# Kernel optimization log

Hardware: AMD Instinct MI355X
Metric: run time of the kernel (lower is better)

## Reference

```python
import jax, jax.numpy as jnp
import numpy as np

NUM_EMBEDDINGS = 1024
EMBEDDING_DIM = 256
COMMITMENT_COST = 0.25
B, C, T = 16, 256, 4096


def setup_inputs() -> dict:
    key = jax.random.key(0)
    k_in, k_cb = jax.random.split(key)
    inputs = jax.random.normal(k_in, (B, C, T), dtype=jnp.float32)
    # matches nn.Embedding init uniform_(-1/K, 1/K)
    codebook = jax.random.uniform(
        k_cb, (NUM_EMBEDDINGS, EMBEDDING_DIM), dtype=jnp.float32,
        minval=-1.0 / NUM_EMBEDDINGS, maxval=1.0 / NUM_EMBEDDINGS)
    return {"inputs": inputs, "codebook": codebook}


def reference(inputs, codebook):
    # inputs: [B, C, T] -> [B, T, C] (channel-last), eval mode (no dead-code swap)
    x = jnp.transpose(inputs, (0, 2, 1))            # [B, T, C]
    flat = x.reshape(-1, EMBEDDING_DIM)             # [N, D]
    distances = (jnp.sum(flat * flat, axis=1, keepdims=True)
                 + jnp.sum(codebook * codebook, axis=1)
                 - 2.0 * jnp.matmul(flat, codebook.T))   # [N, K]
    encoding_indices = jnp.argmin(distances, axis=1)     # [N]
    quantized = codebook[encoding_indices].reshape(x.shape)  # [B, T, C]
    sg = jax.lax.stop_gradient
    e_latent_loss = jnp.mean(jnp.square(sg(quantized) - x))
    q_latent_loss = jnp.mean(jnp.square(quantized - sg(x)))
    vq_loss = e_latent_loss + COMMITMENT_COST * q_latent_loss
    quantized_st = x + sg(quantized - x)                 # straight-through
    quantized_st = jnp.transpose(quantized_st, (0, 2, 1))  # back to [B, C, T]
    indices = encoding_indices.reshape(B, T)
    return quantized_st, vq_loss, indices
```

## Files before the change

kernel.cpp:

```cpp
#include <hip/hip_runtime.h>
#include <stdint.h>

#define DIMS 256
#define NT 4096
#define NROWS 65536
#define THETA 1.5e-4f

typedef float    f32x4_t __attribute__((ext_vector_type(4)));
typedef _Float16 f16x8_t __attribute__((ext_vector_type(8)));
typedef _Float16 f16x4_t __attribute__((ext_vector_type(4)));

__global__ __launch_bounds__(64) void vq_prep(const float* __restrict__ cb,
                                              float* __restrict__ se,
                                              _Float16* __restrict__ cb16){
  __shared__ float sq[256];
  const int k = blockIdx.x;
  const int tid = threadIdx.x;
  float4 v = *(const float4*)(cb + (size_t)k*256 + tid*4);
  f16x4_t p;
  p.x = (_Float16)(v.x * 512.f);
  p.y = (_Float16)(v.y * 512.f);
  p.z = (_Float16)(v.z * 512.f);
  p.w = (_Float16)(v.w * 512.f);
  *(f16x4_t*)(cb16 + (size_t)k*256 + tid*4) = p;
  sq[tid*4+0] = __fmul_rn(v.x, v.x);
  sq[tid*4+1] = __fmul_rn(v.y, v.y);
  sq[tid*4+2] = __fmul_rn(v.z, v.z);
  sq[tid*4+3] = __fmul_rn(v.w, v.w);
  __syncthreads();
  if (tid < 16){
    const int h = tid >> 3, j = tid & 7;
    float r = sq[h*128 + j];
    #pragma unroll
    for (int i = 1; i < 16; ++i) r = __fadd_rn(r, sq[h*128 + j + 8*i]);
    r = __fadd_rn(r, __shfl_xor(r, 1));
    r = __fadd_rn(r, __shfl_xor(r, 2));
    r = __fadd_rn(r, __shfl_xor(r, 4));
    r = __fadd_rn(r, __shfl_xor(r, 8));
    if (tid == 0) se[k] = r;
  }
}


#define AH(r,c)    Ah[(size_t)(r)*264 + (c)]
#define BHL(s,k,c) Bh[((size_t)((s)*256 + (k)))*40 + (c)]
#define QQ(t,c)    q[(size_t)(t)*260 + (c)]

#define T2I(v, i, v1, i1, v2) { \
  bool lt = (v) < (v1); \
  (v2) = lt ? (v1) : fminf((v2), (v)); \
  (i1) = lt ? (i) : (i1); \
  (v1) = lt ? (v) : (v1); }

#define DECL_T2(M,R) \
  float b1_##M##R = 3.4e38f, b2_##M##R = 3.4e38f; int bi_##M##R = 0x7fffffff;

#define FOLD(M,R) { \
  float v; \
  v = fmaf(a##M##0[R], NEGI, ec0); T2I(v, kb +  0, b1_##M##R, bi_##M##R, b2_##M##R); \
  v = fmaf(a##M##1[R], NEGI, ec1); T2I(v, kb + 16, b1_##M##R, bi_##M##R, b2_##M##R); \
  v = fmaf(a##M##2[R], NEGI, ec2); T2I(v, kb + 32, b1_##M##R, bi_##M##R, b2_##M##R); \
  v = fmaf(a##M##3[R], NEGI, ec3); T2I(v, kb + 48, b1_##M##R, bi_##M##R, b2_##M##R); }

#define BSTEP(CC, S) { \
  *(f16x8_t*)&BHL((CC)&1, codeS, cOff)     = rb##S##0; \
  *(f16x8_t*)&BHL((CC)&1, codeS, cOff + 8) = rb##S##1; \
  asm volatile("s_waitcnt lgkmcnt(0)" ::: "memory"); \
  __builtin_amdgcn_s_barrier(); \
  asm volatile("" ::: "memory"); \
  { \
    const int nn = ktb + (CC) + 2; \
    if (nn < 32){ \
      const _Float16* p_ = cb16 + ((size_t)((nn>>3)*256) + codeS)*DIMS + (nn&7)*32 + cOff; \
      rb##S##0 = *(const f16x8_t*)(p_); rb##S##1 = *(const f16x8_t*)(p_ + 8); \
    } \
  } \
  { \
    f16x8_t bh0 = *(const f16x8_t*)&BHL((CC)&1, bC0, fq8); \
    f16x8_t bh1 = *(const f16x8_t*)&BHL((CC)&1, bC1, fq8); \
    f16x8_t bh2 = *(const f16x8_t*)&BHL((CC)&1, bC2, fq8); \
    f16x8_t bh3 = *(const f16x8_t*)&BHL((CC)&1, bC3, fq8); \
    f16x8_t ah0 = *(const f16x8_t*)&AH(wr32 + fr, (CC)*32 + fq8); \
    f16x8_t ah1 = *(const f16x8_t*)&AH(wr32 + 16 + fr, (CC)*32 + fq8); \
    a00 = __builtin_amdgcn_mfma_f32_16x16x32_f16(ah0, bh0, a00, 0, 0, 0); \
    a01 = __builtin_amdgcn_mfma_f32_16x16x32_f16(ah0, bh1, a01, 0, 0, 0); \
    a02 = __builtin_amdgcn_mfma_f32_16x16x32_f16(ah0, bh2, a02, 0, 0, 0); \
    a03 = __builtin_amdgcn_mfma_f32_16x16x32_f16(ah0, bh3, a03, 0, 0, 0); \
    a10 = __builtin_amdgcn_mfma_f32_16x16x32_f16(ah1, bh0, a10, 0, 0, 0); \
    a11 = __builtin_amdgcn_mfma_f32_16x16x32_f16(ah1, bh1, a11, 0, 0, 0); \
    a12 = __builtin_amdgcn_mfma_f32_16x16x32_f16(ah1, bh2, a12, 0, 0, 0); \
    a13 = __builtin_amdgcn_mfma_f32_16x16x32_f16(ah1, bh3, a13, 0, 0, 0); \
  } }

#define MSTEP(MK) { \
  float ov1 = __shfl_xor(v1, MK); int oi1 = __shfl_xor(i1, MK); float ov2 = __shfl_xor(v2, MK); \
  bool tk = ov1 < v1; \
  v2 = tk ? fminf(v1, ov2) : fminf(v2, ov1); \
  i1 = tk ? oi1 : i1; \
  v1 = tk ? ov1 : v1; }

#define MERGE(M,R) { \
  float v1 = b1_##M##R, v2 = b2_##M##R; int i1 = bi_##M##R; \
  MSTEP(1) MSTEP(2) MSTEP(4) MSTEP(8) \
  if (fr == 0) comb[(wr32 + (M)*16 + fq*4 + (R))*4 + wc] = make_float4(v1, __int_as_float(i1), v2, 0.f); }

__global__ __launch_bounds__(512, 1) void vq_scores(
    const float* __restrict__ x, const float* __restrict__ cb,
    const _Float16* __restrict__ cb16, const float* __restrict__ se,
    float* __restrict__ out0, float* __restrict__ out2,
    unsigned* __restrict__ wl, unsigned* __restrict__ cnt, double* __restrict__ accd)
{
  __shared__ __align__(16) char smem[79360];
  _Float16* Ah   = (_Float16*)smem;
  _Float16* Bh   = (_Float16*)(smem + 33792);
  float4*   comb = (float4*)(smem + 74752);
  int*      codeL= (int*)(smem + 78848);
  float*    sxa  = (float*)(smem + 79104);
  float*    q    = (float*)smem;

  const int tid  = threadIdx.x;
  const int lane = tid & 63;
  const int wid  = tid >> 6;
  const int wr   = wid >> 2;
  const int wc   = wid & 3;
  const int fr   = lane & 15;
  const int fq   = lane >> 4;
  const int wr32 = wr * 32;
  const int fq8  = fq * 8;
  const int wcfr = wc*64 + fr;
  const int n0   = blockIdx.x * 64;
  const int bb   = n0 >> 12;
  const int t0   = n0 & 4095;
  const float NEGI = -1.0f/256.0f;

  const int codeS = tid >> 1;
  const int cOff  = (tid & 1) << 4;

  f16x8_t rbA0, rbA1, rbB0, rbB1;
  {
    const _Float16* p_ = cb16 + (size_t)codeS * DIMS + cOff;
    rbA0 = *(const f16x8_t*)(p_); rbA1 = *(const f16x8_t*)(p_ + 8);
  }
  {
    const _Float16* p_ = cb16 + (size_t)codeS * DIMS + 32 + cOff;
    rbB0 = *(const f16x8_t*)(p_); rbB1 = *(const f16x8_t*)(p_ + 8);
  }

  {
    const int dup = tid >> 7;
    const int c4  = tid & 7;
    const int tt  = ((tid >> 3) & 15) << 2;
    #pragma unroll
    for (int cc2 = 0; cc2 < 2; ++cc2){
      const int c0 = (dup*2 + cc2) * 32;
      const float* xp = x + ((size_t)(bb*DIMS + c0 + c4*4))*NT + t0 + tt;
      f32x4_t va0 = __builtin_nontemporal_load((const f32x4_t*)(xp));
      f32x4_t va1 = __builtin_nontemporal_load((const f32x4_t*)(xp + NT));
      f32x4_t va2 = __builtin_nontemporal_load((const f32x4_t*)(xp + 2*NT));
      f32x4_t va3 = __builtin_nontemporal_load((const f32x4_t*)(xp + 3*NT));
      #pragma unroll
      for (int j = 0; j < 4; ++j){
        f16x4_t p;
        p.x = (_Float16)(va0[j]);
        p.y = (_Float16)(va1[j]);
        p.z = (_Float16)(va2[j]);
        p.w = (_Float16)(va3[j]);
        *(f16x4_t*)&AH(tt + j, c0 + c4*4) = p;
      }
    }
  }

  const f32x4_t Z = {0.f, 0.f, 0.f, 0.f};
  f32x4_t a00=Z,a01=Z,a02=Z,a03=Z, a10=Z,a11=Z,a12=Z,a13=Z;
  DECL_T2(0,0) DECL_T2(0,1) DECL_T2(0,2) DECL_T2(0,3)
  DECL_T2(1,0) DECL_T2(1,1) DECL_T2(1,2) DECL_T2(1,3)

  const int bC0 = wc*64 + 0*16 + fr;
  const int bC1 = wc*64 + 1*16 + fr;
  const int bC2 = wc*64 + 2*16 + fr;
  const int bC3 = wc*64 + 3*16 + fr;

  for (int kt = 0; kt < 4; ++kt){
    const int ktb = kt * 8;
    BSTEP(0,A) BSTEP(1,B) BSTEP(2,A) BSTEP(3,B)
    BSTEP(4,A) BSTEP(5,B) BSTEP(6,A) BSTEP(7,B)

    const int kb = kt*256 + wcfr;
    const float ec0 = se[kb], ec1 = se[kb+16], ec2 = se[kb+32], ec3 = se[kb+48];
    FOLD(0,0) FOLD(0,1) FOLD(0,2) FOLD(0,3)
    FOLD(1,0) FOLD(1,1) FOLD(1,2) FOLD(1,3)
    a00=Z;a01=Z;a02=Z;a03=Z; a10=Z;a11=Z;a12=Z;a13=Z;
  }

  MERGE(0,0) MERGE(0,1) MERGE(0,2) MERGE(0,3)
  MERGE(1,0) MERGE(1,1) MERGE(1,2) MERGE(1,3)
  __syncthreads();

  {
    const int row = tid >> 3, seg = tid & 7;
    float s = 0.f;
    #pragma unroll
    for (int k = 0; k < 4; ++k){
      f16x8_t hv = *(const f16x8_t*)&AH(row, seg*32 + k*8);
      #pragma unroll
      for (int e = 0; e < 8; ++e){
        float f = (float)hv[e];
        s = fmaf(f, f, s);
      }
    }
    s += __shfl_xor(s, 1);
    s += __shfl_xor(s, 2);
    s += __shfl_xor(s, 4);
    if (seg == 0) sxa[row] = s;
  }
  __syncthreads();

  if (tid < 64){
    float4 p = comb[tid*4 + 0];
    float v1 = p.x, v2 = p.z;
    int   i1 = __float_as_int(p.y);
    #pragma unroll
    for (int w = 1; w < 4; ++w){
      p = comb[tid*4 + w];
      bool tk = p.x < v1;
      v2 = tk ? fminf(v1, p.z) : fminf(v2, p.x);
      i1 = tk ? __float_as_int(p.y) : i1;
      v1 = tk ? p.x : v1;
    }
    const int r = n0 + tid;
    codeL[tid] = i1;
    out2[r] = (float)i1;
    bool flg = !(v2 - v1 >= THETA);
    if (flg){
      unsigned pos = atomicAdd(cnt, 1u);
      wl[pos] = (unsigned)r;
    }
    double c = flg ? 0.0 : (double)(sxa[tid] + v1);
    #pragma unroll
    for (int m = 1; m < 64; m <<= 1) c += __shfl_xor(c, m);
    if (tid == 0) atomicAdd(accd, c);
  }
  __syncthreads();

  {
    const int r = tid >> 3, seg = tid & 7;
    const float* src = cb + (size_t)codeL[r] * DIMS;
    #pragma unroll
    for (int k = 0; k < 8; ++k){
      float4 v = *(const float4*)(src + k*32 + seg*4);
      *(float4*)&QQ(r, k*32 + seg*4) = v;
    }
  }
  __syncthreads();

  {
    #pragma unroll
    for (int jj = 0; jj < 2; ++jj){
      const int c = wid*32 + jj*16 + (lane >> 2);
      float* dst = out0 + ((size_t)(bb*256 + c))*NT + t0;
      #pragma unroll
      for (int ii = 0; ii < 4; ++ii){
        const int tl = ii*16 + (lane & 3)*4;
        f32x4_t v;
        v[0] = QQ(tl + 0, c);
        v[1] = QQ(tl + 1, c);
        v[2] = QQ(tl + 2, c);
        v[3] = QQ(tl + 3, c);
        __builtin_nontemporal_store(v, (f32x4_t*)(dst + tl));
      }
    }
  }
}

__global__ __launch_bounds__(256) void vq_refine(
    const float* __restrict__ x, const float* __restrict__ cb,
    const float* __restrict__ se,
    const unsigned* __restrict__ wl, const unsigned* __restrict__ cnt,
    float* __restrict__ out2, float* __restrict__ out0, double* __restrict__ accd)
{
  __shared__ float eT[8][1024];
  __shared__ float xs[DIMS][8];
  __shared__ int   rows_s[8];
  __shared__ float sxs[8];
  __shared__ float wv[4][8];
  __shared__ int   wi[4][8];
  __shared__ int   wiF[8];

  const unsigned n = *cnt;
  const unsigned groups = (n + 7u) >> 3;
  const int tid  = threadIdx.x;
  const int lane = tid & 63;
  const int wid  = tid >> 6;

  for (unsigned g = blockIdx.x; g < groups; g += gridDim.x){
    __syncthreads();
    if (tid < 8){
      unsigned e = g*8u + (unsigned)tid;
      rows_s[tid] = (int)wl[e < n ? e : (n - 1u)];
    }
    __syncthreads();
    #pragma unroll
    for (int rep = 0; rep < 8; ++rep){
      int id = rep * 256 + tid;
      int c = id >> 3, r = id & 7;
      int row = rows_s[r];
      xs[c][r] = x[((size_t)((row >> 12)*DIMS + c))*NT + (row & 4095)];
    }
    __syncthreads();
    if (tid < 128){
      const int r = tid >> 4, hj = tid & 15;
      const int h = hj >> 3, j = hj & 7;
      float v0 = xs[h*128 + j][r];
      float s = __fmul_rn(v0, v0);
      #pragma unroll
      for (int i = 1; i < 16; ++i){
        float v = xs[h*128 + j + 8*i][r];
        s = __fadd_rn(s, __fmul_rn(v, v));
      }
      s = __fadd_rn(s, __shfl_xor(s, 1));
      s = __fadd_rn(s, __shfl_xor(s, 2));
      s = __fadd_rn(s, __shfl_xor(s, 4));
      s = __fadd_rn(s, __shfl_xor(s, 8));
      if (hj == 0) sxs[r] = s;
    }

    float s[8][4];
    #pragma unroll
    for (int r = 0; r < 8; ++r)
      #pragma unroll
      for (int u = 0; u < 4; ++u) s[r][u] = 0.f;

    for (int c0 = 0; c0 < DIMS; c0 += 8){
      __syncthreads();
      #pragma unroll
      for (int rep = 0; rep < 8; ++rep){
        int id2 = rep * 256 + tid;
        int k = id2 >> 1, qq = id2 & 1;
        float4 v = *(const float4*)&cb[(size_t)k * DIMS + c0 + qq * 4];
        eT[qq*4 + 0][k] = v.x; eT[qq*4 + 1][k] = v.y;
        eT[qq*4 + 2][k] = v.z; eT[qq*4 + 3][k] = v.w;
      }
      __syncthreads();
      #pragma unroll
      for (int cc = 0; cc < 8; ++cc){
        float4 ev = *(const float4*)&eT[cc][wid*256 + lane*4];
        #pragma unroll
        for (int r = 0; r < 8; ++r){
          float xv = xs[c0 + cc][r];
          s[r][0] = fmaf(xv, ev.x, s[r][0]);
          s[r][1] = fmaf(xv, ev.y, s[r][1]);
          s[r][2] = fmaf(xv, ev.z, s[r][2]);
          s[r][3] = fmaf(xv, ev.w, s[r][3]);
        }
      }
    }

    float4 sek = *(const float4*)&se[wid*256 + lane*4];
    #pragma unroll
    for (int r = 0; r < 8; ++r){
      const float sxv = sxs[r];
      float bv = 3.4e38f; int bi = 0x7fffffff;
      #pragma unroll
      for (int u = 0; u < 4; ++u){
        float d = __fsub_rn(__fadd_rn(sxv, (&sek.x)[u]),
                            __fadd_rn(s[r][u], s[r][u]));
        int k = wid*256 + lane*4 + u;
        if (d < bv || (d == bv && k < bi)) { bv = d; bi = k; }
      }
      #pragma unroll
      for (int m = 1; m < 64; m <<= 1){
        float ov = __shfl_xor(bv, m);
        int   oi = __shfl_xor(bi, m);
        if (ov < bv || (ov == bv && oi < bi)) { bv = ov; bi = oi; }
      }
      if (lane == 0){ wv[wid][r] = bv; wi[wid][r] = bi; }
    }
    __syncthreads();
    if (tid < 8){
      const int r = tid;
      float bv = wv[0][r]; int bi = wi[0][r];
      #pragma unroll
      for (int w = 1; w < 4; ++w){
        float ov = wv[w][r]; int oi = wi[w][r];
        if (ov < bv || (ov == bv && oi < bi)) { bv = ov; bi = oi; }
      }
      wiF[r] = bi;
      if (g*8u + (unsigned)r < n){
        int row = rows_s[r];
        out2[row] = (float)bi;
        atomicAdd(accd, (double)bv);
      }
    }
    __syncthreads();
    #pragma unroll
    for (int r = 0; r < 8; ++r){
      if (g*8u + (unsigned)r < n){
        int row  = rows_s[r];
        int code = wiF[r];
        out0[((size_t)((row >> 12)*256 + tid))*NT + (row & 4095)] = cb[(size_t)code*DIMS + tid];
      }
    }
  }
}

__global__ void vq_final(const double* __restrict__ accd, float* __restrict__ out1){
  *out1 = (float)(1.25 * (*accd) * (1.0 / 16777216.0));
}

extern "C" void kernel_launch(void* const* d_in, const int* in_sizes, int n_in,
                              void* d_out, int out_size, void* d_ws, size_t ws_size,
                              hipStream_t stream)
{
  const float* x  = (const float*)d_in[0];
  const float* cb = (const float*)d_in[1];
  float* out  = (float*)d_out;
  float* out0 = out;
  float* out1 = out + (size_t)16777216;
  float* out2 = out + (size_t)16777217;

  char* ws = (char*)d_ws;
  double*   accd = (double*)(ws + 0);
  unsigned* cnt  = (unsigned*)(ws + 8);
  float*    se   = (float*)(ws + 64);
  unsigned* wl   = (unsigned*)(ws + 4160);
  _Float16* cb16 = (_Float16*)(ws + 266304);

  hipMemsetAsync(d_ws, 0, 16, stream);
  vq_prep  <<<dim3(1024), dim3(64),  0, stream>>>(cb, se, cb16);
  vq_scores<<<dim3(1024), dim3(512), 0, stream>>>(x, cb, cb16, se, out0, out2, wl, cnt, accd);
  vq_refine<<<dim3(512),  dim3(256), 0, stream>>>(x, cb, se, wl, cnt, out2, out0, accd);
  vq_final <<<dim3(1),    dim3(1),   0, stream>>>(accd, out1);
}
```

Baseline: 174.2 us.

## Stream codebook tiles into LDS via global_load_lds with XOR swizzle

Replaces the register-staged codebook pipeline (global load to VGPRs, then ds_write) with direct global-to-LDS DMA loads using an XOR-swizzled, unpadded layout. This shrinks the shared-memory footprint and removes the per-step LDS store plus lgkmcnt wait. The loop becomes a single 32-step loop with a vmcnt wait and barrier per step, and s_setprio raises priority around the MFMA block. The comb buffer is pre-initialised, which adds an extra barrier, and correctness depends on the swizzle and per-wave destination mapping lining up.

```diff
diff --git a/kernel.cpp b/kernel.cpp
--- a/kernel.cpp
+++ b/kernel.cpp
@@ -9,6 +9,10 @@
 typedef float    f32x4_t __attribute__((ext_vector_type(4)));
 typedef _Float16 f16x8_t __attribute__((ext_vector_type(8)));
 typedef _Float16 f16x4_t __attribute__((ext_vector_type(4)));
+
+#define GLDS16(gsrc, ldst) \
+  __builtin_amdgcn_global_load_lds((const __attribute__((address_space(1))) void*)(gsrc), \
+      (__attribute__((address_space(3))) void*)(ldst), 16, 0, 0)
 
 __global__ __launch_bounds__(64) void vq_prep(const float* __restrict__ cb,
                                               float* __restrict__ se,
@@ -43,7 +47,6 @@
 
 
 #define AH(r,c)    Ah[(size_t)(r)*264 + (c)]
-#define BHL(s,k,c) Bh[((size_t)((s)*256 + (k)))*40 + (c)]
 #define QQ(t,c)    q[(size_t)(t)*260 + (c)]
 
 #define T2I(v, i, v1, i1, v2) { \
@@ -62,36 +65,6 @@
   v = fmaf(a##M##2[R], NEGI, ec2); T2I(v, kb + 32, b1_##M##R, bi_##M##R, b2_##M##R); \
   v = fmaf(a##M##3[R], NEGI, ec3); T2I(v, kb + 48, b1_##M##R, bi_##M##R, b2_##M##R); }
 
-#define BSTEP(CC, S) { \
-  *(f16x8_t*)&BHL((CC)&1, codeS, cOff)     = rb##S##0; \
-  *(f16x8_t*)&BHL((CC)&1, codeS, cOff + 8) = rb##S##1; \
-  asm volatile("s_waitcnt lgkmcnt(0)" ::: "memory"); \
-  __builtin_amdgcn_s_barrier(); \
-  asm volatile("" ::: "memory"); \
-  { \
-    const int nn = ktb + (CC) + 2; \
-    if (nn < 32){ \
-      const _Float16* p_ = cb16 + ((size_t)((nn>>3)*256) + codeS)*DIMS + (nn&7)*32 + cOff; \
-      rb##S##0 = *(const f16x8_t*)(p_); rb##S##1 = *(const f16x8_t*)(p_ + 8); \
-    } \
-  } \
-  { \
-    f16x8_t bh0 = *(const f16x8_t*)&BHL((CC)&1, bC0, fq8); \
-    f16x8_t bh1 = *(const f16x8_t*)&BHL((CC)&1, bC1, fq8); \
-    f16x8_t bh2 = *(const f16x8_t*)&BHL((CC)&1, bC2, fq8); \
-    f16x8_t bh3 = *(const f16x8_t*)&BHL((CC)&1, bC3, fq8); \
-    f16x8_t ah0 = *(const f16x8_t*)&AH(wr32 + fr, (CC)*32 + fq8); \
-    f16x8_t ah1 = *(const f16x8_t*)&AH(wr32 + 16 + fr, (CC)*32 + fq8); \
-    a00 = __builtin_amdgcn_mfma_f32_16x16x32_f16(ah0, bh0, a00, 0, 0, 0); \
-    a01 = __builtin_amdgcn_mfma_f32_16x16x32_f16(ah0, bh1, a01, 0, 0, 0); \
-    a02 = __builtin_amdgcn_mfma_f32_16x16x32_f16(ah0, bh2, a02, 0, 0, 0); \
-    a03 = __builtin_amdgcn_mfma_f32_16x16x32_f16(ah0, bh3, a03, 0, 0, 0); \
-    a10 = __builtin_amdgcn_mfma_f32_16x16x32_f16(ah1, bh0, a10, 0, 0, 0); \
-    a11 = __builtin_amdgcn_mfma_f32_16x16x32_f16(ah1, bh1, a11, 0, 0, 0); \
-    a12 = __builtin_amdgcn_mfma_f32_16x16x32_f16(ah1, bh2, a12, 0, 0, 0); \
-    a13 = __builtin_amdgcn_mfma_f32_16x16x32_f16(ah1, bh3, a13, 0, 0, 0); \
-  } }
-
 #define MSTEP(MK) { \
   float ov1 = __shfl_xor(v1, MK); int oi1 = __shfl_xor(i1, MK); float ov2 = __shfl_xor(v2, MK); \
   bool tk = ov1 < v1; \
@@ -110,12 +83,12 @@
     float* __restrict__ out0, float* __restrict__ out2,
     unsigned* __restrict__ wl, unsigned* __restrict__ cnt, double* __restrict__ accd)
 {
-  __shared__ __align__(16) char smem[79360];
+  __shared__ __align__(16) char smem[71168];
   _Float16* Ah   = (_Float16*)smem;
-  _Float16* Bh   = (_Float16*)(smem + 33792);
-  float4*   comb = (float4*)(smem + 74752);
-  int*      codeL= (int*)(smem + 78848);
-  float*    sxa  = (float*)(smem + 79104);
+  char*     BhRaw= smem + 33792;
+  float4*   comb = (float4*)(smem + 66560);
+  int*      codeL= (int*)(smem + 70656);
+  float*    sxa  = (float*)(smem + 70912);
   float*    q    = (float*)smem;
 
   const int tid  = threadIdx.x;
@@ -133,18 +106,25 @@
   const int t0   = n0 & 4095;
   const float NEGI = -1.0f/256.0f;
 
-  const int codeS = tid >> 1;
-  const int cOff  = (tid & 1) << 4;
-
-  f16x8_t rbA0, rbA1, rbB0, rbB1;
-  {
-    const _Float16* p_ = cb16 + (size_t)codeS * DIMS + cOff;
-    rbA0 = *(const f16x8_t*)(p_); rbA1 = *(const f16x8_t*)(p_ + 8);
-  }
-  {
-    const _Float16* p_ = cb16 + (size_t)codeS * DIMS + 32 + cOff;
-    rbB0 = *(const f16x8_t*)(p_); rbB1 = *(const f16x8_t*)(p_ + 8);
-  }
+  const int cA = wid*32 + (lane >> 2);
+  const int cB = cA + 16;
+  const int qA = (lane & 3) ^ ((cA >> 1) & 3);
+  const int qB = (lane & 3) ^ ((cB >> 1) & 3);
+  const char* cbB = (const char*)cb16;
+  const size_t srcA = (size_t)cA*512 + qA*16;
+  const size_t srcB = (size_t)cB*512 + qB*16;
+  char* dstA = BhRaw + wid*2048;
+  char* dstB = dstA + 1024;
+
+  int bOff[4];
+  #pragma unroll
+  for (int cf = 0; cf < 4; ++cf){
+    const int cd = wc*64 + cf*16 + fr;
+    bOff[cf] = cd*64 + ((fq ^ ((cd >> 1) & 3)) << 4);
+  }
+
+  GLDS16(cbB + srcA, dstA);
+  GLDS16(cbB + srcB, dstB);
 
   {
     const int dup = tid >> 7;
@@ -169,27 +149,55 @@
       }
     }
   }
+  comb[(tid >> 2)*4 + (tid & 3)] = make_float4(3.4e38f, __int_as_float(0x7fffffff), 3.4e38f, 0.f);
 
   const f32x4_t Z = {0.f, 0.f, 0.f, 0.f};
   f32x4_t a00=Z,a01=Z,a02=Z,a03=Z, a10=Z,a11=Z,a12=Z,a13=Z;
   DECL_T2(0,0) DECL_T2(0,1) DECL_T2(0,2) DECL_T2(0,3)
   DECL_T2(1,0) DECL_T2(1,1) DECL_T2(1,2) DECL_T2(1,3)
 
-  const int bC0 = wc*64 + 0*16 + fr;
-  const int bC1 = wc*64 + 1*16 + fr;
-  const int bC2 = wc*64 + 2*16 + fr;
-  const int bC3 = wc*64 + 3*16 + fr;
-
-  for (int kt = 0; kt < 4; ++kt){
-    const int ktb = kt * 8;
-    BSTEP(0,A) BSTEP(1,B) BSTEP(2,A) BSTEP(3,B)
-    BSTEP(4,A) BSTEP(5,B) BSTEP(6,A) BSTEP(7,B)
-
-    const int kb = kt*256 + wcfr;
-    const float ec0 = se[kb], ec1 = se[kb+16], ec2 = se[kb+32], ec3 = se[kb+48];
-    FOLD(0,0) FOLD(0,1) FOLD(0,2) FOLD(0,3)
-    FOLD(1,0) FOLD(1,1) FOLD(1,2) FOLD(1,3)
-    a00=Z;a01=Z;a02=Z;a03=Z; a10=Z;a11=Z;a12=Z;a13=Z;
+  __syncthreads();
+
+  for (int p = 0; p < 32; ++p){
+    if (p){
+      asm volatile("s_waitcnt vmcnt(0)" ::: "memory");
+      __builtin_amdgcn_s_barrier();
+      asm volatile("" ::: "memory");
+    }
+    const int nn = p + 1;
+    if (nn < 32){
+      const char* g = cbB + (size_t)(nn >> 3)*131072 + (size_t)(nn & 7)*64;
+      char* d = (nn & 1) ? (dstA + 16384) : dstA;
+      GLDS16(g + srcA, d);
+      GLDS16(g + srcB, d + 1024);
+    }
+    {
+      const char* bbuf = BhRaw + ((p & 1) << 14);
+      f16x8_t bh0 = *(const f16x8_t*)(bbuf + bOff[0]);
+      f16x8_t bh1 = *(const f16x8_t*)(bbuf + bOff[1]);
+      f16x8_t bh2 = *(const f16x8_t*)(bbuf + bOff[2]);
+      f16x8_t bh3 = *(const f16x8_t*)(bbuf + bOff[3]);
+      const int cc = p & 7;
+      f16x8_t ah0 = *(const f16x8_t*)&AH(wr32 + fr, cc*32 + fq8);
+      f16x8_t ah1 = *(const f16x8_t*)&AH(wr32 + 16 + fr, cc*32 + fq8);
+      __builtin_amdgcn_s_setprio(1);
+      a00 = __builtin_amdgcn_mfma_f32_16x16x32_f16(ah0, bh0, a00, 0, 0, 0);
+      a01 = __builtin_amdgcn_mfma_f32_16x16x32_f16(ah0, bh1, a01, 0, 0, 0);
+      a02 = __builtin_amdgcn_mfma_f32_16x16x32_f16(ah0, bh2, a02, 0, 0, 0);
+      a03 = __builtin_amdgcn_mfma_f32_16x16x32_f16(ah0, bh3, a03, 0, 0, 0);
+      a10 = __builtin_amdgcn_mfma_f32_16x16x32_f16(ah1, bh0, a10, 0, 0, 0);
+      a11 = __builtin_amdgcn_mfma_f32_16x16x32_f16(ah1, bh1, a11, 0, 0, 0);
+      a12 = __builtin_amdgcn_mfma_f32_16x16x32_f16(ah1, bh2, a12, 0, 0, 0);
+      a13 = __builtin_amdgcn_mfma_f32_16x16x32_f16(ah1, bh3, a13, 0, 0, 0);
+      __builtin_amdgcn_s_setprio(0);
+    }
+    if ((p & 7) == 7){
+      const int kb = (p >> 3)*256 + wcfr;
+      const float ec0 = se[kb], ec1 = se[kb+16], ec2 = se[kb+32], ec3 = se[kb+48];
+      FOLD(0,0) FOLD(0,1) FOLD(0,2) FOLD(0,3)
+      FOLD(1,0) FOLD(1,1) FOLD(1,2) FOLD(1,3)
+      a00=Z;a01=Z;a02=Z;a03=Z; a10=Z;a11=Z;a12=Z;a13=Z;
+    }
   }
 
   MERGE(0,0) MERGE(0,1) MERGE(0,2) MERGE(0,3)
@@ -216,16 +224,16 @@
   __syncthreads();
 
   if (tid < 64){
-    float4 p = comb[tid*4 + 0];
-    float v1 = p.x, v2 = p.z;
-    int   i1 = __float_as_int(p.y);
+    float4 pv = comb[tid*4 + 0];
+    float v1 = pv.x, v2 = pv.z;
+    int   i1 = __float_as_int(pv.y);
     #pragma unroll
     for (int w = 1; w < 4; ++w){
-      p = comb[tid*4 + w];
-      bool tk = p.x < v1;
-      v2 = tk ? fminf(v1, p.z) : fminf(v2, p.x);
-      i1 = tk ? __float_as_int(p.y) : i1;
-      v1 = tk ? p.x : v1;
+      pv = comb[tid*4 + w];
+      bool tk = pv.x < v1;
+      v2 = tk ? fminf(v1, pv.z) : fminf(v2, pv.x);
+      i1 = tk ? __float_as_int(pv.y) : i1;
+      v1 = tk ? pv.x : v1;
     }
     const int r = n0 + tid;
     codeL[tid] = i1;
```

New measurement: 159.6 us. 1.09x faster.
